# Kernel tuning notes

Hardware: AMD Instinct MI355X
Metric: run time of the kernel (lower is better)

The kernel has to match this reference:

```python
import jax, jax.numpy as jnp
import numpy as np

N, DIM, H, D = 8192, 1152, 16, 72
SEGS = 4  # equal-length image segments


def setup_inputs() -> dict:
    key = jax.random.key(0)
    ks = jax.random.split(key, 8)
    s = 0.02
    return {
        "hidden_states": jax.random.normal(ks[0], (N, DIM), jnp.float32),
        "cos": jax.random.uniform(ks[1], (N, D), jnp.float32, -1.0, 1.0),
        "sin": jax.random.uniform(ks[2], (N, D), jnp.float32, -1.0, 1.0),
        "cu_seqlens": (jnp.arange(SEGS + 1, dtype=jnp.int32) * (N // SEGS)),
        "w_qkv": jax.random.normal(ks[3], (DIM, 3 * DIM), jnp.float32) * s,
        "b_qkv": jax.random.normal(ks[4], (3 * DIM,), jnp.float32) * s,
        "w_proj": jax.random.normal(ks[5], (DIM, DIM), jnp.float32) * s,
        "b_proj": jax.random.normal(ks[6], (DIM,), jnp.float32) * s,
    }


def _rope(x, cos, sin):
    # x: [N, H, D]; cos/sin: [N, 1, D]
    half = x.shape[-1] // 2
    x1, x2 = x[..., :half], x[..., half:]
    rot = jnp.concatenate([-x2, x1], axis=-1)
    return x * cos + rot * sin


def reference(hidden_states, cos, sin, cu_seqlens, w_qkv, b_qkv, w_proj, b_proj):
    n = hidden_states.shape[0]
    qkv = (hidden_states @ w_qkv + b_qkv).reshape(n, 3, H, D)
    q, k, v = qkv[:, 0], qkv[:, 1], qkv[:, 2]
    c = cos[:, None, :]
    s = sin[:, None, :]
    q = _rope(q, c, s)
    k = _rope(k, c, s)
    # equal-length segments derived statically from cu_seqlens
    segs = int(cu_seqlens.shape[0]) - 1
    L = n // segs
    qs = q.reshape(segs, L, H, D)
    ks = k.reshape(segs, L, H, D)
    vs = v.reshape(segs, L, H, D)
    scale = D ** -0.5
    scores = jnp.einsum("slhd,smhd->shlm", qs, ks) * scale
    attn = jax.nn.softmax(scores, axis=-1)
    out = jnp.einsum("shlm,smhd->slhd", attn, vs).reshape(n, DIM)
    return out @ w_proj + b_proj
```

## Files before the change

### kernel.cpp

```cpp
#include <hip/hip_runtime.h>
#include <hip/hip_bf16.h>
#include <cstdint>
#include <cstddef>

typedef __bf16 bf16;
typedef __attribute__((ext_vector_type(4))) __bf16 bf16x4;
typedef __attribute__((ext_vector_type(8))) __bf16 bf16x8;
typedef __attribute__((ext_vector_type(4))) float f32x4;
typedef __attribute__((ext_vector_type(16))) float f32x16;
typedef __attribute__((ext_vector_type(4))) float floatx4;
typedef __attribute__((ext_vector_type(2))) unsigned uint2_t;
typedef __attribute__((ext_vector_type(4))) unsigned uint4_t;

#define NTOK 8192
#define DIMM 1152
#define NH   16
#define HD   72
#define SEGS 4
#define SEGL 2048

__device__ __forceinline__ void gload16(const void* gsrc, void* ldst) {
  __builtin_amdgcn_global_load_lds(
      (const __attribute__((address_space(1))) void*)gsrc,
      (__attribute__((address_space(3))) void*)ldst,
      16, 0, 0);
}

__device__ __forceinline__ unsigned cvtpk(float a, float b) {
  unsigned r;
  asm volatile("v_cvt_pk_bf16_f32 %0, %1, %2" : "=v"(r) : "v"(a), "v"(b));
  return r;
}

__global__ __launch_bounds__(256) void k_prep(const float* __restrict__ hs,
                                              bf16* __restrict__ hsb,
                                              const float* __restrict__ wq,
                                              bf16* __restrict__ wqT,
                                              const float* __restrict__ wp,
                                              bf16* __restrict__ wpT) {
  __shared__ bf16 tile[64][73];
  const int b = blockIdx.x, t = threadIdx.x;
  if (b < 4608) {
    int i = b * 256 + t;
    const floatx4* s = (const floatx4*)hs + (size_t)i * 2;
    floatx4 a = s[0], c = s[1];
    uint4_t o;
    o[0] = cvtpk(a.x, a.y);
    o[1] = cvtpk(a.z, a.w);
    o[2] = cvtpk(c.x, c.y);
    o[3] = cvtpk(c.z, c.w);
    *((uint4_t*)hsb + i) = o;
    return;
  }
  const float* src; bf16* dst; int R, C, bx, by;
  if (b < 4608 + 1008) {
    int idx = b - 4608;
    src = wq; dst = wqT; R = 1152; C = 3456; bx = idx % 56; by = idx / 56;
  } else {
    int idx = b - 5616;
    src = wp; dst = wpT; R = 1152; C = 1152; bx = idx % 18; by = idx / 18;
  }
  int bc = bx * 64, br = by * 64;
#pragma unroll
  for (int i = 0; i < 16; i++) {
    int idx = i * 256 + t;
    int r = idx >> 6, c = idx & 63;
    float v = (bc + c < C) ? src[(size_t)(br + r) * C + bc + c] : 0.f;
    tile[c][r] = (bf16)v;
  }
  __syncthreads();
#pragma unroll
  for (int i = 0; i < 16; i++) {
    int idx = i * 256 + t;
    int r = idx >> 6, c = idx & 63;
    dst[(size_t)(bc + r) * R + br + c] = tile[r][c];
  }
}

#define QPHASE(D, CH, KK, READB, STG, VM)                                      \
  {                                                                            \
    asm volatile("s_waitcnt vmcnt(" VM ")" ::: "memory");                      \
    __builtin_amdgcn_s_barrier();                                              \
    __builtin_amdgcn_sched_barrier(0);                                         \
    bf16x8 av[4];                                                              \
    _Pragma("unroll")                                                          \
    for (int mi = 0; mi < 4; mi++)                                             \
      av[mi] = *(const bf16x8*)&sA[D][wr][(CH * 64 + mi * 16 + lr) * 64 + ga[KK]]; \
    if (READB) {                                                               \
      _Pragma("unroll")                                                        \
      for (int ni = 0; ni < 4; ni++)                                           \
        bv[ni] = *(const bf16x8*)&sB[D][bh][(bro + ni * 16 + lr) * 64 + ga[KK]]; \
    }                                                                          \
    asm volatile("s_waitcnt lgkmcnt(0)" ::: "memory");                         \
    __builtin_amdgcn_sched_barrier(0);                                         \
    STG;                                                                       \
    __builtin_amdgcn_s_setprio(1);                                             \
    _Pragma("unroll")                                                          \
    for (int mi = 0; mi < 4; mi++)                                             \
      _Pragma("unroll")                                                        \
      for (int ni = 0; ni < 4; ni++)                                           \
        acc[CH * 4 + mi][ni] = __builtin_amdgcn_mfma_f32_16x16x32_bf16(        \
            av[mi], bv[ni], acc[CH * 4 + mi][ni], 0, 0, 0);                    \
    __builtin_amdgcn_s_setprio(0);                                             \
  }

__global__ __launch_bounds__(512, 2) void k_gemm8p(const bf16* __restrict__ A,
                                                   const bf16* __restrict__ Bt,
                                                   const float* __restrict__ bias,
                                                   bf16* __restrict__ Cout,
                                                   int M, int Nreal, int K, int gx) {
  __shared__ bf16 sA[2][2][128 * 64];
  __shared__ bf16 sB[2][2][128 * 64];
  const int t = threadIdx.x, wave = t >> 6, lane = t & 63;
  const int lr = lane & 15, lg = lane >> 4;
  const int nwg = gridDim.x, bid = blockIdx.x;
  const int swz = (bid & 7) * (nwg >> 3) + (bid >> 3);
  const int bx = swz % gx, by = swz / gx;
  const int m0 = by * 256, n0 = bx * 256;
  const int wr = wave >> 2, wc = wave & 3;
  const int bh = wc >> 1, bro = (wc & 1) * 64;
  const int NS = K >> 6;

  f32x4 acc[8][4];
#pragma unroll
  for (int i = 0; i < 8; i++)
#pragma unroll
    for (int j = 0; j < 4; j++)
#pragma unroll
      for (int q = 0; q < 4; q++) acc[i][j][q] = 0.f;

  const bf16* Ab = A + (size_t)m0 * K;
  const bf16* Bb = Bt + (size_t)n0 * K;
  const int glsw8 = (((t & 7) ^ ((t >> 3) & 7)) * 8);
  const bf16* Asrc[2][2];
  const bf16* Bsrc[2][2];
#pragma unroll
  for (int h = 0; h < 2; h++)
#pragma unroll
    for (int p = 0; p < 2; p++) {
      Asrc[h][p] = Ab + (size_t)(h * 128 + p * 64 + (t >> 3)) * K + glsw8;
      Bsrc[h][p] = Bb + (size_t)(h * 128 + p * 64 + (t >> 3)) * K + glsw8;
    }
  auto STA = [&](int d2, int h, int ttt) {
    gload16(Asrc[h][0] + (size_t)ttt * 64, (char*)&sA[d2][h][0] + t * 16);
    gload16(Asrc[h][1] + (size_t)ttt * 64, (char*)&sA[d2][h][0] + 8192 + t * 16);
  };
  auto STB = [&](int d2, int h, int ttt) {
    gload16(Bsrc[h][0] + (size_t)ttt * 64, (char*)&sB[d2][h][0] + t * 16);
    gload16(Bsrc[h][1] + (size_t)ttt * 64, (char*)&sB[d2][h][0] + 8192 + t * 16);
  };
  const int ga[2] = { ((0 + lg) ^ (lr & 7)) * 8, ((4 + lg) ^ (lr & 7)) * 8 };

  STB(0, 0, 0);
  STB(0, 1, 0);
  STA(0, 0, 0);
  STA(0, 1, 0);
  STB(1, 0, 1);

  bf16x8 bv[4];
  int tt = 0;
  for (; tt < NS - 1; ++tt) {
    const int d = tt & 1, dn = d ^ 1;
    QPHASE(d, 0, 0, true,  { STB(dn, 1, tt + 1); }, "4");
    QPHASE(d, 1, 0, false, { STA(dn, 0, tt + 1); }, "4");
    QPHASE(d, 0, 1, true,  { STA(dn, 1, tt + 1); }, "6");
    QPHASE(d, 1, 1, false, { if (tt + 2 < NS) STB(d, 0, tt + 2); }, "6");
  }
  {
    const int d = tt & 1;
    QPHASE(d, 0, 0, true,  {;}, "0");
    QPHASE(d, 1, 0, false, {;}, "0");
    QPHASE(d, 0, 1, true,  {;}, "0");
    QPHASE(d, 1, 1, false, {;}, "0");
  }

#pragma unroll
  for (int mi = 0; mi < 8; ++mi)
#pragma unroll
    for (int ni = 0; ni < 4; ++ni) {
      int col = n0 + wc * 64 + ni * 16 + lr;
      if (col < Nreal) {
        float bc_ = bias[col];
#pragma unroll
        for (int j = 0; j < 4; j++) {
          int row = m0 + wr * 128 + mi * 16 + lg * 4 + j;
          Cout[(size_t)row * Nreal + col] = (bf16)(acc[mi][ni][j] + bc_);
        }
      }
    }
}

template <int BM, int BN, int MI, int NI, int THREADS, bool OUT_F32, int MW>
__global__ __launch_bounds__(THREADS, MW) void k_gemmP(const bf16* __restrict__ A,
                                                       const bf16* __restrict__ Bt,
                                                       const float* __restrict__ bias,
                                                       void* __restrict__ Cout,
                                                       int M, int Nreal, int K, int gx) {
  __shared__ bf16 sA[3][BM * 32];
  __shared__ bf16 sB[3][BN * 32];
  constexpr int WN = BN / (NI * 16);
  constexpr int nA = (BM * 4) / THREADS;
  constexpr int nB = (BN * 4) / THREADS;
  constexpr int NLD = nA + nB;
  static_assert(NLD == 3 || NLD == 4 || NLD == 6, "vmcnt literal");
  const int t = threadIdx.x, wave = t >> 6, lane = t & 63;
  const int lr = lane & 15, lg = lane >> 4;
  const int nwg = gridDim.x, bid = blockIdx.x;
  const int swz = (bid & 7) * (nwg >> 3) + (bid >> 3);
  const int bx = swz % gx, by = swz / gx;
  const int m0 = by * BM, n0 = bx * BN;
  const int wr = wave / WN, wc = wave % WN;
  const int NS = K >> 5;

  f32x4 acc[MI][NI];
#pragma unroll
  for (int i = 0; i < MI; i++)
#pragma unroll
    for (int j = 0; j < NI; j++)
#pragma unroll
      for (int q = 0; q < 4; q++) acc[i][j][q] = 0.f;

  const bf16* Ab = A + (size_t)m0 * K;
  const bf16* Bb = Bt + (size_t)n0 * K;
  const int glsw = ((t & 3) ^ ((t >> 3) & 3)) * 8;
  const int rbase = t >> 2;

  auto STAGE = [&](int slot, int k0) {
#pragma unroll
    for (int p = 0; p < nA; ++p)
      gload16(Ab + (size_t)(rbase + p * (THREADS / 4)) * K + k0 + glsw,
              (char*)&sA[slot][0] + p * (THREADS * 16) + wave * 1024);
#pragma unroll
    for (int p = 0; p < nB; ++p)
      gload16(Bb + (size_t)(rbase + p * (THREADS / 4)) * K + k0 + glsw,
              (char*)&sB[slot][0] + p * (THREADS * 16) + wave * 1024);
  };

  const int swz4 = (lr >> 1) & 3;
  const int aoff = (wr * MI * 16 + lr) * 32 + ((lg ^ swz4) * 8);
  const int boff = (wc * NI * 16 + lr) * 32 + ((lg ^ swz4) * 8);

  STAGE(0, 0);
  STAGE(1, 32);

  int slot = 0;
  for (int j = 0; j < NS; ++j) {
    if (j == NS - 1) {
      asm volatile("s_waitcnt vmcnt(0)" ::: "memory");
    } else if constexpr (NLD == 3) {
      asm volatile("s_waitcnt vmcnt(3)" ::: "memory");
    } else if constexpr (NLD == 4) {
      asm volatile("s_waitcnt vmcnt(4)" ::: "memory");
    } else {
      asm volatile("s_waitcnt vmcnt(6)" ::: "memory");
    }
    __builtin_amdgcn_s_barrier();
    __builtin_amdgcn_sched_barrier(0);
    bf16x8 av[MI], bv[NI];
#pragma unroll
    for (int mi = 0; mi < MI; mi++)
      av[mi] = *(const bf16x8*)&sA[slot][aoff + mi * 512];
#pragma unroll
    for (int ni = 0; ni < NI; ni++)
      bv[ni] = *(const bf16x8*)&sB[slot][boff + ni * 512];
    asm volatile("s_waitcnt lgkmcnt(0)" ::: "memory");
    __builtin_amdgcn_sched_barrier(0);
    if (j + 2 < NS) {
      int s2 = slot + 2; if (s2 >= 3) s2 -= 3;
      STAGE(s2, (j + 2) * 32);
    }
    __builtin_amdgcn_s_setprio(1);
#pragma unroll
    for (int mi = 0; mi < MI; mi++)
#pragma unroll
      for (int ni = 0; ni < NI; ni++)
        acc[mi][ni] = __builtin_amdgcn_mfma_f32_16x16x32_bf16(av[mi], bv[ni], acc[mi][ni], 0, 0, 0);
    __builtin_amdgcn_s_setprio(0);
    if (++slot == 3) slot = 0;
  }

#pragma unroll
  for (int mi = 0; mi < MI; ++mi)
#pragma unroll
    for (int ni = 0; ni < NI; ++ni) {
      int col = n0 + wc * NI * 16 + ni * 16 + lr;
      if (col < Nreal) {
        float bc_ = bias[col];
#pragma unroll
        for (int j = 0; j < 4; j++) {
          int row = m0 + wr * MI * 16 + mi * 16 + lg * 4 + j;
          float v = acc[mi][ni][j] + bc_;
          if (OUT_F32)
            ((float*)Cout)[(size_t)row * Nreal + col] = v;
          else
            ((bf16*)Cout)[(size_t)row * Nreal + col] = (bf16)v;
        }
      }
    }
}

__global__ __launch_bounds__(256) void k_ropev(const bf16* __restrict__ qkv,
                                               const float* __restrict__ cs,
                                               const float* __restrict__ sn,
                                               bf16* __restrict__ Qp,
                                               bf16* __restrict__ Kp,
                                               bf16* __restrict__ Vt) {
  __shared__ bf16 tl[64][80];
  const int bid = blockIdx.x, t = threadIdx.x;
  if (bid < 2048) {
    const float QS = 0.17002323f;
    const int n0 = bid * 4;
#pragma unroll
    for (int it = 0; it < 6; ++it) {
      int idx = it * 256 + t;
      int tok = idx / 384;
      int r = idx - tok * 384;
      int which = r / 192;
      int r2 = r - which * 192;
      int h = r2 / 12;
      int d0 = (r2 - h * 12) * 8;
      int n = n0 + tok;
      bf16* dst = which ? Kp : Qp;
      size_t ob = ((((size_t)((n >> 11) * NH + h)) * 3 + (d0 >> 5)) * SEGL +
                   (n & 2047)) * 32 + (d0 & 31);
      if (d0 >= HD) {
        uint4_t z = {0u, 0u, 0u, 0u};
        *(uint4_t*)&dst[ob] = z;
        continue;
      }
      const bf16* rowp = qkv + (size_t)n * (3 * DIMM) + which * DIMM + h * HD;
      bf16x8 xv = *(const bf16x8*)&rowp[d0];
      float ov[8];
      if (d0 == 32) {
        bf16x4 a = *(const bf16x4*)&rowp[68];
        bf16x4 b = *(const bf16x4*)&rowp[0];
#pragma unroll
        for (int j = 0; j < 4; j++) { ov[j] = -(float)a[j]; ov[j + 4] = (float)b[j]; }
      } else if (d0 < 32) {
        bf16x4 a = *(const bf16x4*)&rowp[d0 + 36];
        bf16x4 b = *(const bf16x4*)&rowp[d0 + 40];
#pragma unroll
        for (int j = 0; j < 4; j++) { ov[j] = -(float)a[j]; ov[j + 4] = -(float)b[j]; }
      } else {
        bf16x4 a = *(const bf16x4*)&rowp[d0 - 36];
        bf16x4 b = *(const bf16x4*)&rowp[d0 - 32];
#pragma unroll
        for (int j = 0; j < 4; j++) { ov[j] = (float)a[j]; ov[j + 4] = (float)b[j]; }
      }
      const float* cr = cs + (size_t)n * HD + d0;
      const float* sr = sn + (size_t)n * HD + d0;
      floatx4 c0 = *(const floatx4*)cr, c1 = *(const floatx4*)(cr + 4);
      floatx4 s0 = *(const floatx4*)sr, s1 = *(const floatx4*)(sr + 4);
      float vv[8];
#pragma unroll
      for (int j = 0; j < 4; j++) {
        vv[j] = (float)xv[j] * c0[j] + ov[j] * s0[j];
        vv[j + 4] = (float)xv[j + 4] * c1[j] + ov[j + 4] * s1[j];
      }
      if (!which) {
#pragma unroll
        for (int j = 0; j < 8; j++) vv[j] *= QS;
      }
      uint4_t w;
      w[0] = cvtpk(vv[0], vv[1]);
      w[1] = cvtpk(vv[2], vv[3]);
      w[2] = cvtpk(vv[4], vv[5]);
      w[3] = cvtpk(vv[6], vv[7]);
      *(uint4_t*)&dst[ob] = w;
    }
  } else {
    int idx2 = bid - 2048;
    int s = idx2 >> 9, h = (idx2 >> 5) & 15, l0 = (idx2 & 31) * 64;
    for (int idx = t; idx < 64 * HD; idx += 256) {
      int l = idx / HD, d = idx - l * HD;
      tl[l][d] = qkv[(size_t)(s * SEGL + l0 + l) * (3 * DIMM) + 2 * DIMM + h * HD + d];
    }
    __syncthreads();
    for (int idx = t; idx < 96 * 64; idx += 256) {
      int d = idx >> 6, l = idx & 63;
      bf16 v = (d < HD) ? tl[l][d] : ((d == HD) ? (bf16)1.f : (bf16)0.f);
      Vt[((size_t)(s * NH + h) * 96 + d) * SEGL + l0 + l] = v;
    }
  }
}

__global__ __launch_bounds__(256, 2) void k_attn(const bf16* __restrict__ Qg,
                                                 const bf16* __restrict__ Kg,
                                                 const bf16* __restrict__ Vg,
                                                 bf16* __restrict__ Oo) {
  __shared__ bf16 sK[2][3 * 64 * 32];
  __shared__ bf16 sV[2][96 * 64];
  const int t = threadIdx.x, wave = t >> 6, lane = t & 63;
  const int c = lane & 31, hi = lane >> 5;
  const int bid = blockIdx.x;
  const int g = ((bid >> 6) << 3) | (bid & 7);
  const int qt = (bid >> 3) & 7;
  const int s = g >> 4, h = g & 15, q0 = qt * 256;
  const bf16* Qb = Qg + (size_t)(s * NH + h) * 3 * SEGL * 32;
  const bf16* Kb = Kg + (size_t)(s * NH + h) * 3 * SEGL * 32;
  const bf16* Vb = Vg + (size_t)(s * NH + h) * 96 * SEGL;

  const bf16* kq[3];
  const bf16* vq[3];
#pragma unroll
  for (int i = 0; i < 3; i++) {
    int ch = wave * 3 + i;
    int kk = ch >> 2;
    int r = (ch & 3) * 16 + (lane >> 2);
    int gg = (lane & 3) ^ ((r >> 1) & 3);
    kq[i] = Kb + (size_t)kk * (SEGL * 32) + (size_t)r * 32 + gg * 8;
    int rv = ch * 8 + (lane >> 3);
    int gv = (lane & 7) ^ (rv & 7);
    vq[i] = Vb + (size_t)rv * SEGL + gv * 8;
  }

  bf16x8 Qf[2][5];
#pragma unroll
  for (int sni = 0; sni < 2; sni++)
#pragma unroll
    for (int kk = 0; kk < 5; kk++) {
      int qr = q0 + wave * 64 + sni * 32 + c;
      Qf[sni][kk] = *(const bf16x8*)&Qb[(size_t)(kk >> 1) * (SEGL * 32) +
                                        (size_t)qr * 32 + ((kk & 1) * 2 + hi) * 8];
    }

#pragma unroll
  for (int i = 0; i < 3; i++) {
    gload16(kq[i], (char*)sK[0] + (wave * 3 + i) * 1024);
    gload16(vq[i], (char*)sV[0] + (wave * 3 + i) * 1024);
    kq[i] += 2048;
    vq[i] += 64;
  }
  __syncthreads();

  f32x16 accO[3][2];
#pragma unroll
  for (int df = 0; df < 3; df++)
#pragma unroll
    for (int sni = 0; sni < 2; sni++)
#pragma unroll
      for (int r = 0; r < 16; r++) accO[df][sni][r] = 0.f;
  f32x16 ZC;
#pragma unroll
  for (int r = 0; r < 16; r++) ZC[r] = 0.f;

  int cur = 0;
  for (int tile = 0; tile < 32; ++tile) {
    if (tile + 1 < 32) {
#pragma unroll
      for (int i = 0; i < 3; i++) {
        gload16(kq[i], (char*)sK[cur ^ 1] + (wave * 3 + i) * 1024);
        gload16(vq[i], (char*)sV[cur ^ 1] + (wave * 3 + i) * 1024);
        kq[i] += 2048;
        vq[i] += 64;
      }
    }

    f32x16 S[2][2];
    __builtin_amdgcn_s_setprio(1);
#pragma unroll
    for (int kk = 0; kk < 5; kk++) {
      bf16x8 Kf[2];
#pragma unroll
      for (int smi = 0; smi < 2; smi++) {
        int kr = smi * 32 + c;
        int gg = (((kk & 1) * 2 + hi) ^ ((kr >> 1) & 3));
        Kf[smi] = *(const bf16x8*)&sK[cur][(kk >> 1) * 2048 + kr * 32 + gg * 8];
      }
#pragma unroll
      for (int smi = 0; smi < 2; smi++)
#pragma unroll
        for (int sni = 0; sni < 2; sni++)
          S[smi][sni] = __builtin_amdgcn_mfma_f32_32x32x16_bf16(
              Kf[smi], Qf[sni][kk], kk ? S[smi][sni] : ZC, 0, 0, 0);
    }
    __builtin_amdgcn_s_setprio(0);

    __builtin_amdgcn_s_setprio(1);
#pragma unroll
    for (int kk = 0; kk < 4; kk++) {
      bf16x8 Vf[3];
#pragma unroll
      for (int df = 0; df < 3; df++) {
        int dr = df * 32 + c;
        int gg = ((kk * 2 + hi) ^ (dr & 7));
        Vf[df] = *(const bf16x8*)&sV[cur][dr * 64 + gg * 8];
      }
#pragma unroll
      for (int sni = 0; sni < 2; sni++) {
        const int smi = kk >> 1;
        const int base = (kk & 1) * 8;
        unsigned u0 = cvtpk(__builtin_amdgcn_exp2f(S[smi][sni][base + 0]),
                            __builtin_amdgcn_exp2f(S[smi][sni][base + 1]));
        unsigned u1 = cvtpk(__builtin_amdgcn_exp2f(S[smi][sni][base + 2]),
                            __builtin_amdgcn_exp2f(S[smi][sni][base + 3]));
        unsigned u2 = cvtpk(__builtin_amdgcn_exp2f(S[smi][sni][base + 4]),
                            __builtin_amdgcn_exp2f(S[smi][sni][base + 5]));
        unsigned u3 = cvtpk(__builtin_amdgcn_exp2f(S[smi][sni][base + 6]),
                            __builtin_amdgcn_exp2f(S[smi][sni][base + 7]));
        asm volatile("v_permlane32_swap_b32 %0, %1" : "+v"(u0), "+v"(u2));
        asm volatile("v_permlane32_swap_b32 %0, %1" : "+v"(u1), "+v"(u3));
        union { bf16x8 v; unsigned u[4]; } pb;
        pb.u[0] = u0; pb.u[1] = u1; pb.u[2] = u2; pb.u[3] = u3;
#pragma unroll
        for (int df = 0; df < 3; df++)
          accO[df][sni] = __builtin_amdgcn_mfma_f32_32x32x16_bf16(Vf[df], pb.v, accO[df][sni], 0, 0, 0);
      }
    }
    __builtin_amdgcn_s_setprio(0);

    __syncthreads();
    cur ^= 1;
  }

#pragma unroll
  for (int sni = 0; sni < 2; sni++) {
    float lown = accO[2][sni][4];
    float lv = lown + __shfl_xor(lown, 32, 64);
    float inv = 1.f / lv;
    int token = s * SEGL + q0 + wave * 64 + sni * 32 + c;
#pragma unroll
    for (int df = 0; df < 3; df++)
#pragma unroll
      for (int rg = 0; rg < 4; rg++) {
        int d0 = df * 32 + rg * 8 + hi * 4;
        if (d0 < HD) {
          uint2_t w;
          w[0] = cvtpk(accO[df][sni][rg * 4 + 0] * inv, accO[df][sni][rg * 4 + 1] * inv);
          w[1] = cvtpk(accO[df][sni][rg * 4 + 2] * inv, accO[df][sni][rg * 4 + 3] * inv);
          *(uint2_t*)&Oo[(size_t)token * DIMM + h * HD + d0] = w;
        }
      }
  }
}

extern "C" void kernel_launch(void* const* d_in, const int* in_sizes, int n_in,
                              void* d_out, int out_size, void* d_ws, size_t ws_size,
                              hipStream_t stream) {
  (void)in_sizes; (void)n_in; (void)out_size; (void)ws_size;
  const float* hs     = (const float*)d_in[0];
  const float* cosp   = (const float*)d_in[1];
  const float* sinp   = (const float*)d_in[2];
  const float* w_qkv  = (const float*)d_in[4];
  const float* b_qkv  = (const float*)d_in[5];
  const float* w_proj = (const float*)d_in[6];
  const float* b_proj = (const float*)d_in[7];
  float* out = (float*)d_out;

  char* ws = (char*)d_ws;
  bf16* hsb    = (bf16*)(ws + 0);
  bf16* wprojT = (bf16*)(ws + 26836992);
  bf16* qkv    = (bf16*)(ws + 29491200);
  bf16* Qp     = (bf16*)(ws + 86114304);
  bf16* Kp     = (bf16*)(ws + 111280128);
  bf16* Vt     = (bf16*)(ws + 136445952);
  bf16* ao     = (bf16*)(ws + 161611776);
  bf16* wqkvT  = (bf16*)(ws + 161611776);

  k_prep<<<5940, 256, 0, stream>>>(hs, hsb, w_qkv, wqkvT, w_proj, wprojT);
  k_gemm8p<<<448, 512, 0, stream>>>(hsb, wqkvT, b_qkv, qkv, 8192, 3456, 1152, 14);
  k_ropev<<<4096, 256, 0, stream>>>(qkv, cosp, sinp, Qp, Kp, Vt);
  k_attn<<<512, 256, 0, stream>>>(Qp, Kp, Vt, ao);
  k_gemmP<128, 128, 4, 4, 256, true, 3><<<576, 256, 0, stream>>>(
      ao, wprojT, b_proj, (void*)out, 8192, 1152, 1152, 9);
}
```

Before: 249.5 us.

## Restructure QKV GEMM main loop with full-tile prefetch and staged LDS reads

Replaces the four-phase interleaved QKV GEMM loop, which issued per-half global loads between MFMA groups, with a simpler schedule. The new loop prefetches two whole K-tiles up front, reads LDS fragments in two batches with partial lgkmcnt waits so MFMAs start before all reads land, then issues the next full tile's global loads after a trailing barrier. The aim is fewer barriers and waits per K-step and better overlap of LDS reads with MFMA work. The cost is an extra barrier per iteration and bulk global-load issue instead of spreading it across phases, which may expose memory latency.

```diff
diff --git a/kernel.cpp b/kernel.cpp
--- a/kernel.cpp
+++ b/kernel.cpp
@@ -77,38 +77,11 @@
   }
 }
 
-#define QPHASE(D, CH, KK, READB, STG, VM)                                      \
-  {                                                                            \
-    asm volatile("s_waitcnt vmcnt(" VM ")" ::: "memory");                      \
-    __builtin_amdgcn_s_barrier();                                              \
-    __builtin_amdgcn_sched_barrier(0);                                         \
-    bf16x8 av[4];                                                              \
-    _Pragma("unroll")                                                          \
-    for (int mi = 0; mi < 4; mi++)                                             \
-      av[mi] = *(const bf16x8*)&sA[D][wr][(CH * 64 + mi * 16 + lr) * 64 + ga[KK]]; \
-    if (READB) {                                                               \
-      _Pragma("unroll")                                                        \
-      for (int ni = 0; ni < 4; ni++)                                           \
-        bv[ni] = *(const bf16x8*)&sB[D][bh][(bro + ni * 16 + lr) * 64 + ga[KK]]; \
-    }                                                                          \
-    asm volatile("s_waitcnt lgkmcnt(0)" ::: "memory");                         \
-    __builtin_amdgcn_sched_barrier(0);                                         \
-    STG;                                                                       \
-    __builtin_amdgcn_s_setprio(1);                                             \
-    _Pragma("unroll")                                                          \
-    for (int mi = 0; mi < 4; mi++)                                             \
-      _Pragma("unroll")                                                        \
-      for (int ni = 0; ni < 4; ni++)                                           \
-        acc[CH * 4 + mi][ni] = __builtin_amdgcn_mfma_f32_16x16x32_bf16(        \
-            av[mi], bv[ni], acc[CH * 4 + mi][ni], 0, 0, 0);                    \
-    __builtin_amdgcn_s_setprio(0);                                             \
-  }
-
-__global__ __launch_bounds__(512, 2) void k_gemm8p(const bf16* __restrict__ A,
-                                                   const bf16* __restrict__ Bt,
-                                                   const float* __restrict__ bias,
-                                                   bf16* __restrict__ Cout,
-                                                   int M, int Nreal, int K, int gx) {
+__global__ __launch_bounds__(512, 2) void k_gemmF(const bf16* __restrict__ A,
+                                                  const bf16* __restrict__ Bt,
+                                                  const float* __restrict__ bias,
+                                                  bf16* __restrict__ Cout,
+                                                  int M, int Nreal, int K, int gx) {
   __shared__ bf16 sA[2][2][128 * 64];
   __shared__ bf16 sB[2][2][128 * 64];
   const int t = threadIdx.x, wave = t >> 6, lane = t & 63;
@@ -151,27 +124,82 @@
   };
   const int ga[2] = { ((0 + lg) ^ (lr & 7)) * 8, ((4 + lg) ^ (lr & 7)) * 8 };
 
-  STB(0, 0, 0);
-  STB(0, 1, 0);
-  STA(0, 0, 0);
-  STA(0, 1, 0);
-  STB(1, 0, 1);
-
-  bf16x8 bv[4];
-  int tt = 0;
-  for (; tt < NS - 1; ++tt) {
-    const int d = tt & 1, dn = d ^ 1;
-    QPHASE(d, 0, 0, true,  { STB(dn, 1, tt + 1); }, "4");
-    QPHASE(d, 1, 0, false, { STA(dn, 0, tt + 1); }, "4");
-    QPHASE(d, 0, 1, true,  { STA(dn, 1, tt + 1); }, "6");
-    QPHASE(d, 1, 1, false, { if (tt + 2 < NS) STB(d, 0, tt + 2); }, "6");
-  }
-  {
+  STB(0, 0, 0); STB(0, 1, 0); STA(0, 0, 0); STA(0, 1, 0);
+  STB(1, 0, 1); STB(1, 1, 1); STA(1, 0, 1); STA(1, 1, 1);
+
+  for (int tt = 0; tt < NS; ++tt) {
     const int d = tt & 1;
-    QPHASE(d, 0, 0, true,  {;}, "0");
-    QPHASE(d, 1, 0, false, {;}, "0");
-    QPHASE(d, 0, 1, true,  {;}, "0");
-    QPHASE(d, 1, 1, false, {;}, "0");
+    if (tt + 1 < NS) {
+      asm volatile("s_waitcnt vmcnt(8)" ::: "memory");
+    } else {
+      asm volatile("s_waitcnt vmcnt(0)" ::: "memory");
+    }
+    __builtin_amdgcn_s_barrier();
+    __builtin_amdgcn_sched_barrier(0);
+    bf16x8 av0[4], av1[4], av2[4], av3[4], bv0[4], bv1[4];
+#pragma unroll
+    for (int mi = 0; mi < 4; mi++)
+      av0[mi] = *(const bf16x8*)&sA[d][wr][(mi * 16 + lr) * 64 + ga[0]];
+#pragma unroll
+    for (int ni = 0; ni < 4; ni++)
+      bv0[ni] = *(const bf16x8*)&sB[d][bh][(bro + ni * 16 + lr) * 64 + ga[0]];
+#pragma unroll
+    for (int mi = 0; mi < 4; mi++)
+      av1[mi] = *(const bf16x8*)&sA[d][wr][(64 + mi * 16 + lr) * 64 + ga[0]];
+    asm volatile("s_waitcnt lgkmcnt(4)" ::: "memory");
+    __builtin_amdgcn_sched_barrier(0);
+    __builtin_amdgcn_s_setprio(1);
+#pragma unroll
+    for (int mi = 0; mi < 4; mi++)
+#pragma unroll
+      for (int ni = 0; ni < 4; ni++)
+        acc[mi][ni] = __builtin_amdgcn_mfma_f32_16x16x32_bf16(av0[mi], bv0[ni], acc[mi][ni], 0, 0, 0);
+    __builtin_amdgcn_s_setprio(0);
+    __builtin_amdgcn_sched_barrier(0);
+#pragma unroll
+    for (int mi = 0; mi < 4; mi++)
+      av2[mi] = *(const bf16x8*)&sA[d][wr][(mi * 16 + lr) * 64 + ga[1]];
+#pragma unroll
+    for (int ni = 0; ni < 4; ni++)
+      bv1[ni] = *(const bf16x8*)&sB[d][bh][(bro + ni * 16 + lr) * 64 + ga[1]];
+#pragma unroll
+    for (int mi = 0; mi < 4; mi++)
+      av3[mi] = *(const bf16x8*)&sA[d][wr][(64 + mi * 16 + lr) * 64 + ga[1]];
+    asm volatile("s_waitcnt lgkmcnt(12)" ::: "memory");
+    __builtin_amdgcn_sched_barrier(0);
+    __builtin_amdgcn_s_setprio(1);
+#pragma unroll
+    for (int mi = 0; mi < 4; mi++)
+#pragma unroll
+      for (int ni = 0; ni < 4; ni++)
+        acc[4 + mi][ni] = __builtin_amdgcn_mfma_f32_16x16x32_bf16(av1[mi], bv0[ni], acc[4 + mi][ni], 0, 0, 0);
+    __builtin_amdgcn_s_setprio(0);
+    __builtin_amdgcn_sched_barrier(0);
+    asm volatile("s_waitcnt lgkmcnt(4)" ::: "memory");
+    __builtin_amdgcn_sched_barrier(0);
+    __builtin_amdgcn_s_setprio(1);
+#pragma unroll
+    for (int mi = 0; mi < 4; mi++)
+#pragma unroll
+      for (int ni = 0; ni < 4; ni++)
+        acc[mi][ni] = __builtin_amdgcn_mfma_f32_16x16x32_bf16(av2[mi], bv1[ni], acc[mi][ni], 0, 0, 0);
+    __builtin_amdgcn_s_setprio(0);
+    __builtin_amdgcn_sched_barrier(0);
+    asm volatile("s_waitcnt lgkmcnt(0)" ::: "memory");
+    __builtin_amdgcn_sched_barrier(0);
+    __builtin_amdgcn_s_setprio(1);
+#pragma unroll
+    for (int mi = 0; mi < 4; mi++)
+#pragma unroll
+      for (int ni = 0; ni < 4; ni++)
+        acc[4 + mi][ni] = __builtin_amdgcn_mfma_f32_16x16x32_bf16(av3[mi], bv1[ni], acc[4 + mi][ni], 0, 0, 0);
+    __builtin_amdgcn_s_setprio(0);
+    __builtin_amdgcn_s_barrier();
+    __builtin_amdgcn_sched_barrier(0);
+    if (tt + 2 < NS) {
+      STB(d, 0, tt + 2); STB(d, 1, tt + 2);
+      STA(d, 0, tt + 2); STA(d, 1, tt + 2);
+    }
   }
 
 #pragma unroll
@@ -558,7 +586,7 @@
   bf16* wqkvT  = (bf16*)(ws + 161611776);
 
   k_prep<<<5940, 256, 0, stream>>>(hs, hsb, w_qkv, wqkvT, w_proj, wprojT);
-  k_gemm8p<<<448, 512, 0, stream>>>(hsb, wqkvT, b_qkv, qkv, 8192, 3456, 1152, 14);
+  k_gemmF<<<448, 512, 0, stream>>>(hsb, wqkvT, b_qkv, qkv, 8192, 3456, 1152, 14);
   k_ropev<<<4096, 256, 0, stream>>>(qkv, cosp, sinp, Qp, Kp, Vt);
   k_attn<<<512, 256, 0, stream>>>(Qp, Kp, Vt, ao);
   k_gemmP<128, 128, 4, 4, 256, true, 3><<<576, 256, 0, stream>>>(
```

Measured after the change: 251.1 us. Within noise of the previous version (+0.7%).
